# Performance work log

Hardware: AMD Instinct MI355X
Metric: run time of the kernel (lower is better)

The kernel has to match this reference:

```python
import jax, jax.numpy as jnp
import numpy as np

B, N, D, S, H = 64, 4096, 256, 8, 256
ITERS = 3
EPS = 1e-8
SCALE = D ** -0.5


def _ln(x, g, b):
    m = jnp.mean(x, axis=-1, keepdims=True)
    v = jnp.mean((x - m) ** 2, axis=-1, keepdims=True)
    return (x - m) * jax.lax.rsqrt(v + 1e-5) * g + b


def setup_inputs() -> dict:
    key = jax.random.key(0)
    ks = jax.random.split(key, 12)
    s = 0.02
    return {
        'inputs': jax.random.normal(ks[0], (B, N, D), jnp.float32),
        'slot_noise': jax.random.normal(ks[1], (B, S, D), jnp.float32),
        'slots_mean': jax.random.normal(ks[2], (1, 1, D), jnp.float32),
        'slots_logvar': s * jax.random.normal(ks[3], (1, 1, D), jnp.float32),
        'Wq': s * jax.random.normal(ks[4], (D, D), jnp.float32),
        'bq': jnp.zeros((D,), jnp.float32),
        'Wk': s * jax.random.normal(ks[5], (D, D), jnp.float32),
        'bk': jnp.zeros((D,), jnp.float32),
        'Wv': s * jax.random.normal(ks[6], (D, D), jnp.float32),
        'bv': jnp.zeros((D,), jnp.float32),
        'W_ih': s * jax.random.normal(ks[7], (3 * D, D), jnp.float32),
        'b_ih': jnp.zeros((3 * D,), jnp.float32),
        'W_hh': s * jax.random.normal(ks[8], (3 * D, D), jnp.float32),
        'b_hh': jnp.zeros((3 * D,), jnp.float32),
        'W1': s * jax.random.normal(ks[9], (H, D), jnp.float32),
        'b1': jnp.zeros((H,), jnp.float32),
        'W2': s * jax.random.normal(ks[10], (D, H), jnp.float32),
        'b2': jnp.zeros((D,), jnp.float32),
        'g_in': jnp.ones((D,), jnp.float32),
        'bias_in': jnp.zeros((D,), jnp.float32),
        'g_slots': jnp.ones((D,), jnp.float32),
        'bias_slots': jnp.zeros((D,), jnp.float32),
        'g_ff': jnp.ones((D,), jnp.float32),
        'bias_ff': jnp.zeros((D,), jnp.float32),
    }


def reference(inputs, slot_noise, slots_mean, slots_logvar, Wq, bq, Wk, bk, Wv, bv,
              W_ih, b_ih, W_hh, b_hh, W1, b1, W2, b2,
              g_in, bias_in, g_slots, bias_slots, g_ff, bias_ff):
    # slot init: mean + exp(logvar) * noise  (exp(logvar) used as multiplier, as in source)
    slots = slots_mean + jnp.exp(slots_logvar) * slot_noise  # [B,S,D]
    x = _ln(inputs, g_in, bias_in)                            # [B,N,D]
    k = x @ Wk.T + bk
    v = x @ Wv.T + bv
    attn = None
    for _ in range(ITERS):
        slots_prev = slots
        sn = _ln(slots, g_slots, bias_slots)
        q = sn @ Wq.T + bq                                    # [B,S,D]
        dots = jnp.einsum('bid,bjd->bij', q, k) * SCALE       # [B,S,N]
        attn = jax.nn.softmax(dots, axis=1) + EPS             # softmax over slots, no renorm
        updates = jnp.einsum('bjd,bij->bid', v, attn)         # [B,S,D]
        # GRUCell (PyTorch convention)
        gi = updates @ W_ih.T + b_ih                          # [B,S,3D]
        gh = slots_prev @ W_hh.T + b_hh
        i_r, i_z, i_n = jnp.split(gi, 3, axis=-1)
        h_r, h_z, h_n = jnp.split(gh, 3, axis=-1)
        r = jax.nn.sigmoid(i_r + h_r)
        z = jax.nn.sigmoid(i_z + h_z)
        n = jnp.tanh(i_n + r * h_n)
        slots = (1.0 - z) * n + z * slots_prev
        # MLP residual
        sf = _ln(slots, g_ff, bias_ff)
        slots = slots + (jax.nn.relu(sf @ W1.T + b1) @ W2.T + b2)
    return (slots, attn)
```

## Files before the change

kernel.cpp:

```cpp
#include <hip/hip_runtime.h>

typedef unsigned short u16;
typedef __bf16 bf16x8 __attribute__((ext_vector_type(8)));
typedef float f32x4 __attribute__((ext_vector_type(4)));

#define DEV static __device__ __forceinline__

DEV u16 f2bf(float f) {
    unsigned int u = __builtin_bit_cast(unsigned int, f);
    u += 0x7FFFu + ((u >> 16) & 1u);
    return (u16)(u >> 16);
}

DEV bf16x8 frag_ld(const u16* p) {
    return __builtin_bit_cast(bf16x8, *(const uint4*)p);
}

DEV float sigm(float x) { return 1.f / (1.f + __expf(-x)); }

DEV float blo(unsigned u) { return __builtin_bit_cast(float, u << 16); }
DEV float bhi(unsigned u) { return __builtin_bit_cast(float, u & 0xffff0000u); }

__global__ __launch_bounds__(256) void kSetup(
    const float* __restrict__ noise, const float* __restrict__ mean,
    const float* __restrict__ logv, float* __restrict__ slots,
    const float* __restrict__ Wq, const float* __restrict__ Wk,
    const float* __restrict__ bq, const float* __restrict__ bk,
    float* __restrict__ Wqk, float* __restrict__ wbc,
    const float* __restrict__ Wv,  float* __restrict__ WvT,
    const float* __restrict__ Wih, float* __restrict__ WihT,
    const float* __restrict__ Whh, float* __restrict__ WhhT,
    const float* __restrict__ W1,  float* __restrict__ W1T,
    const float* __restrict__ W2,  float* __restrict__ W2T)
{
    __shared__ float tile[32][33];
    const int bid = blockIdx.x, t = threadIdx.x;
    if (bid < 512) {
        const int id = bid * 256 + t;
        const int d = id & 255;
        slots[id] = mean[d] + __expf(logv[d]) * noise[id];
        return;
    }
    if (bid < 770) {
        const int a = bid - 512, e = t;
        if (a < 256) {
            float acc = 0.f;
            for (int d = 0; d < 256; ++d) acc += Wq[(size_t)d * 256 + a] * Wk[(size_t)d * 256 + e];
            Wqk[(size_t)a * 256 + e] = acc;
        } else if (a == 256) {
            float acc = 0.f;
            for (int d = 0; d < 256; ++d) acc += bq[d] * Wk[(size_t)d * 256 + e];
            wbc[e] = acc;
        } else {
            float acc = 0.f;
            for (int d = 0; d < 256; ++d) acc += Wq[(size_t)d * 256 + e] * bk[d];
            wbc[256 + e] = acc;
            if (e == 0) {
                float c0 = 0.f;
                for (int d = 0; d < 256; ++d) c0 += bq[d] * bk[d];
                wbc[512] = c0;
            }
        }
        return;
    }
    const int rb = bid - 770;
    const float* in; float* outp; int R, k;
    if (rb < 64)       { in = Wv;  outp = WvT;  R = 256; k = rb; }
    else if (rb < 256) { in = Wih; outp = WihT; R = 768; k = rb - 64; }
    else if (rb < 448) { in = Whh; outp = WhhT; R = 768; k = rb - 256; }
    else if (rb < 512) { in = W1;  outp = W1T;  R = 256; k = rb - 448; }
    else               { in = W2;  outp = W2T;  R = 256; k = rb - 512; }
    const int bx = k & 7, by = k >> 3;
    const int tx = t & 31, ty = t >> 5;
    const int c0 = bx * 32, r0 = by * 32;
    #pragma unroll
    for (int i = 0; i < 4; ++i)
        tile[ty + i * 8][tx] = in[(size_t)(r0 + ty + i * 8) * 256 + c0 + tx];
    __syncthreads();
    #pragma unroll
    for (int i = 0; i < 4; ++i)
        outp[(size_t)(c0 + ty + i * 8) * R + r0 + tx] = tile[tx][ty + i * 8];
}

__global__ __launch_bounds__(256) void kSn(
    const float* __restrict__ slots, const float* __restrict__ gs, const float* __restrict__ bs,
    const float* __restrict__ Wqk, const float* __restrict__ wbc,
    u16* __restrict__ qo, float* __restrict__ qc)
{
    __shared__ float SN[8][256];
    __shared__ float red2[4][8][64];
    const int t = threadIdx.x;
    const int b = blockIdx.y, seg = blockIdx.x;
    const int w = t >> 6, lane = t & 63;
    #pragma unroll
    for (int rr = 0; rr < 2; ++rr) {
        const int r = w * 2 + rr;
        const int c = lane * 4;
        const float4 x = *(const float4*)(slots + ((size_t)b * 8 + r) * 256 + c);
        float s1 = x.x + x.y + x.z + x.w;
        float s2 = x.x * x.x + x.y * x.y + x.z * x.z + x.w * x.w;
        #pragma unroll
        for (int o = 32; o > 0; o >>= 1) { s1 += __shfl_xor(s1, o); s2 += __shfl_xor(s2, o); }
        const float mu = s1 * (1.f / 256.f);
        const float rs = rsqrtf(s2 * (1.f / 256.f) - mu * mu + 1e-5f);
        const float4 g4 = *(const float4*)(gs + c);
        const float4 b4 = *(const float4*)(bs + c);
        SN[r][c + 0] = (x.x - mu) * rs * g4.x + b4.x;
        SN[r][c + 1] = (x.y - mu) * rs * g4.y + b4.y;
        SN[r][c + 2] = (x.z - mu) * rs * g4.z + b4.z;
        SN[r][c + 3] = (x.w - mu) * rs * g4.w + b4.w;
    }
    __syncthreads();
    const int c = seg * 64 + (t & 63);
    const int p = t >> 6;
    float acc[8] = {};
    #pragma unroll 4
    for (int d = p * 64; d < p * 64 + 64; ++d) {
        const float wq = Wqk[(size_t)d * 256 + c];
        #pragma unroll
        for (int r = 0; r < 8; ++r) acc[r] += wq * SN[r][d];
    }
    #pragma unroll
    for (int r = 0; r < 8; ++r) red2[p][r][t & 63] = acc[r];
    __syncthreads();
    const float bb = wbc[c];
    #pragma unroll
    for (int rr = t >> 6; rr < 8; rr += 4) {
        const float s = red2[0][rr][t & 63] + red2[1][rr][t & 63]
                      + red2[2][rr][t & 63] + red2[3][rr][t & 63];
        qo[((size_t)b * 16 + rr) * 256 + c] = f2bf((s + bb) * 0.0625f);
    }
    if (seg == 0) {
        const int r = t >> 5, l = t & 31;
        float a = 0.f;
        #pragma unroll
        for (int d8 = 0; d8 < 8; ++d8) a += SN[r][l * 8 + d8] * wbc[256 + l * 8 + d8];
        #pragma unroll
        for (int o = 16; o > 0; o >>= 1) a += __shfl_xor(a, o);
        if (l == 0) qc[(size_t)b * 8 + r] = 0.0625f * (a + wbc[512]);
    }
}

template<int FUSE>
__global__ __launch_bounds__(256, 2) void kF(
    const float* __restrict__ X,
    const float* __restrict__ gin, const float* __restrict__ bin,
    const u16* __restrict__ Q,
    const float* __restrict__ qcg,
    u16* __restrict__ XN,
    float* __restrict__ attn_out,
    float* __restrict__ part,
    float* __restrict__ part2,
    int write_attn)
{
    __shared__ __align__(16) float att32[128][8];
    __shared__ float usred[4][8][256];
    __shared__ float sred[4][2][4][16];
    const int tid = threadIdx.x;
    const int w = tid >> 6, lane = tid & 63;
    const int quad = lane >> 4, l16 = lane & 15;
    const int dsg = lane & 31, jg = lane >> 5;
    const int b = blockIdx.y, nt = blockIdx.x;
    const int j0 = nt << 8;
    const size_t rowbase = (size_t)b * 4096 + j0;

    const u16* qb = Q + (size_t)b * 16 * 256;
    bf16x8 qfrag[8];
    #pragma unroll
    for (int k0 = 0; k0 < 8; ++k0)
        qfrag[k0] = frag_ld(qb + l16 * 256 + k0 * 32 + quad * 8);

    float c8[8];
    #pragma unroll
    for (int i = 0; i < 8; ++i) c8[i] = qcg[(size_t)b * 8 + i];

    float4 g4, b4;
    if (FUSE) {
        const int cc = lane << 2;
        g4 = *(const float4*)(gin + cc);
        b4 = *(const float4*)(bin + cc);
    }

    float acc[8][8];
    #pragma unroll
    for (int i = 0; i < 8; ++i)
        #pragma unroll
        for (int e = 0; e < 8; ++e) acc[i][e] = 0.f;
    float sacc[4] = {};

    const u16* xb = XN + rowbase * 256;
    const int qb1 = (quad & 1) << 2;

    for (int st = 0; st < 2; ++st) {
        if (FUSE) {
            const int cc = lane << 2;
            #pragma unroll 4
            for (int i = 0; i < 32; ++i) {
                const size_t gr = rowbase + st * 128 + w * 32 + i;
                const float4 x = *(const float4*)(X + gr * 256 + cc);
                float s1 = x.x + x.y + x.z + x.w;
                float s2 = x.x * x.x + x.y * x.y + x.z * x.z + x.w * x.w;
                #pragma unroll
                for (int o = 32; o > 0; o >>= 1) { s1 += __shfl_xor(s1, o); s2 += __shfl_xor(s2, o); }
                const float mu = s1 * (1.f / 256.f);
                const float rs = rsqrtf(s2 * (1.f / 256.f) - mu * mu + 1e-5f);
                ushort4 pk;
                pk.x = f2bf((x.x - mu) * rs * g4.x + b4.x);
                pk.y = f2bf((x.y - mu) * rs * g4.y + b4.y);
                pk.z = f2bf((x.z - mu) * rs * g4.z + b4.z);
                pk.w = f2bf((x.w - mu) * rs * g4.w + b4.w);
                *(ushort4*)(XN + gr * 256 + cc) = pk;
            }
            asm volatile("s_waitcnt vmcnt(0)" ::: "memory");
        }
        f32x4 dacc[2] = {};
        #pragma unroll
        for (int n2 = 0; n2 < 2; ++n2) {
            const int jsl = w * 32 + n2 * 16 + l16;
            const u16* xrow = xb + ((size_t)(st * 128 + jsl)) * 256;
            #pragma unroll
            for (int k0 = 0; k0 < 8; ++k0) {
                const bf16x8 bfr = frag_ld(xrow + k0 * 32 + quad * 8);
                dacc[n2] = __builtin_amdgcn_mfma_f32_16x16x32_bf16(
                    qfrag[k0], bfr, dacc[n2], 0, 0, 0);
            }
        }
        #pragma unroll
        for (int n2 = 0; n2 < 2; ++n2) {
            const int jsl = w * 32 + n2 * 16 + l16;
            float v[8];
            #pragma unroll
            for (int r = 0; r < 4; ++r) {
                v[qb1 + r]       = dacc[n2][r];
                v[(qb1 ^ 4) + r] = __shfl_xor(dacc[n2][r], 16);
            }
            #pragma unroll
            for (int i = 0; i < 8; ++i) v[i] += c8[i];
            float m = v[0];
            #pragma unroll
            for (int i = 1; i < 8; ++i) m = fmaxf(m, v[i]);
            float s = 0.f;
            #pragma unroll
            for (int i = 0; i < 8; ++i) { v[i] = __expf(v[i] - m); s += v[i]; }
            const float inv = 1.f / s;
            if (quad < 2) {
                float4 av;
                av.x = v[qb1 + 0] * inv + 1e-8f;
                av.y = v[qb1 + 1] * inv + 1e-8f;
                av.z = v[qb1 + 2] * inv + 1e-8f;
                av.w = v[qb1 + 3] * inv + 1e-8f;
                sacc[0] += av.x; sacc[1] += av.y; sacc[2] += av.z; sacc[3] += av.w;
                *(float4*)&att32[jsl][qb1] = av;
                if (write_attn) {
                    attn_out[((size_t)b * 8 + qb1 + 0) * 4096 + j0 + st * 128 + jsl] = av.x;
                    attn_out[((size_t)b * 8 + qb1 + 1) * 4096 + j0 + st * 128 + jsl] = av.y;
                    attn_out[((size_t)b * 8 + qb1 + 2) * 4096 + j0 + st * 128 + jsl] = av.z;
                    attn_out[((size_t)b * 8 + qb1 + 3) * 4096 + j0 + st * 128 + jsl] = av.w;
                }
            }
        }
        #pragma unroll 4
        for (int jj = 0; jj < 16; ++jj) {
            const int jsl = w * 32 + jj * 2 + jg;
            const uint4 raw = *(const uint4*)(xb + ((size_t)(st * 128 + jsl)) * 256 + dsg * 8);
            const float4 a0 = *(const float4*)&att32[jsl][0];
            const float4 a1 = *(const float4*)&att32[jsl][4];
            float xf[8];
            xf[0] = blo(raw.x); xf[1] = bhi(raw.x);
            xf[2] = blo(raw.y); xf[3] = bhi(raw.y);
            xf[4] = blo(raw.z); xf[5] = bhi(raw.z);
            xf[6] = blo(raw.w); xf[7] = bhi(raw.w);
            #pragma unroll
            for (int e = 0; e < 8; ++e) {
                acc[0][e] = fmaf(a0.x, xf[e], acc[0][e]);
                acc[1][e] = fmaf(a0.y, xf[e], acc[1][e]);
                acc[2][e] = fmaf(a0.z, xf[e], acc[2][e]);
                acc[3][e] = fmaf(a0.w, xf[e], acc[3][e]);
                acc[4][e] = fmaf(a1.x, xf[e], acc[4][e]);
                acc[5][e] = fmaf(a1.y, xf[e], acc[5][e]);
                acc[6][e] = fmaf(a1.z, xf[e], acc[6][e]);
                acc[7][e] = fmaf(a1.w, xf[e], acc[7][e]);
            }
        }
    }

    #pragma unroll
    for (int i = 0; i < 8; ++i)
        #pragma unroll
        for (int e = 0; e < 8; ++e) acc[i][e] += __shfl_xor(acc[i][e], 32);
    if (jg == 0) {
        #pragma unroll
        for (int i = 0; i < 8; ++i) {
            float4 lo, hi;
            lo.x = acc[i][0]; lo.y = acc[i][1]; lo.z = acc[i][2]; lo.w = acc[i][3];
            hi.x = acc[i][4]; hi.y = acc[i][5]; hi.z = acc[i][6]; hi.w = acc[i][7];
            *(float4*)&usred[w][i][dsg * 8]     = lo;
            *(float4*)&usred[w][i][dsg * 8 + 4] = hi;
        }
    }
    if (quad < 2) {
        #pragma unroll
        for (int r = 0; r < 4; ++r) sred[w][quad][r][l16] = sacc[r];
    }
    __syncthreads();
    #pragma unroll
    for (int i = 0; i < 8; ++i) {
        const float s = usred[0][i][tid] + usred[1][i][tid]
                      + usred[2][i][tid] + usred[3][i][tid];
        part[(((size_t)nt * 64 + b) * 8 + i) * 256 + tid] = s;
    }
    if (tid < 8) {
        const int q = tid >> 2, r = tid & 3;
        float s = 0.f;
        #pragma unroll
        for (int ww = 0; ww < 4; ++ww)
            #pragma unroll
            for (int l = 0; l < 16; ++l) s += sred[ww][q][r][l];
        part2[((size_t)nt * 64 + b) * 8 + tid] = s;
    }
}

__global__ __launch_bounds__(256) void kB3(
    const float* __restrict__ part, const float* __restrict__ part2,
    const float* __restrict__ WvT, const float* __restrict__ bv,
    const float* __restrict__ sl_in,
    const float* __restrict__ WihT, const float* __restrict__ bih,
    const float* __restrict__ WhhT, const float* __restrict__ bhh,
    const float* __restrict__ W1T, const float* __restrict__ b1,
    const float* __restrict__ W2T, const float* __restrict__ b2,
    const float* __restrict__ gf, const float* __restrict__ bff,
    float* __restrict__ sl_out)
{
    __shared__ float Ul[2][256], Sl[2][256];
    __shared__ float red[2][4][6][256];
    __shared__ float SNl[2][256];
    __shared__ float cw[2][2][4];
    __shared__ float Ssl[2];
    const int t = threadIdx.x;
    const int kp = t >> 6, c = t & 63;
    const int row0 = blockIdx.x * 2;

    #pragma unroll
    for (int r = 0; r < 2; ++r) {
        const int row = row0 + r;
        const int b = row >> 3, s = row & 7;
        float u = 0.f;
        #pragma unroll
        for (int nt = 0; nt < 16; ++nt)
            u += part[(((size_t)nt * 64 + b) * 8 + s) * 256 + t];
        Ul[r][t] = u;
        Sl[r][t] = sl_in[(size_t)row * 256 + t];
    }
    if (t < 2) {
        const int row = row0 + t;
        const int b = row >> 3, s = row & 7;
        float ss = 0.f;
        #pragma unroll
        for (int nt = 0; nt < 16; ++nt) ss += part2[((size_t)nt * 64 + b) * 8 + s];
        Ssl[t] = ss;
    }
    __syncthreads();

    {
        float va[2][4] = {};
        #pragma unroll 4
        for (int dd = 0; dd < 64; ++dd) {
            const int d = kp * 64 + dd;
            const float* wr = WvT + (size_t)d * 256;
            const float u0 = Ul[0][d], u1 = Ul[1][d];
            #pragma unroll
            for (int cg = 0; cg < 4; ++cg) {
                const float wv = wr[cg * 64 + c];
                va[0][cg] += wv * u0;
                va[1][cg] += wv * u1;
            }
        }
        #pragma unroll
        for (int r = 0; r < 2; ++r)
            #pragma unroll
            for (int cg = 0; cg < 4; ++cg)
                red[r][kp][0][cg * 64 + c] = va[r][cg];
    }
    __syncthreads();
    const float bvt = bv[t];
    float upd2[2];
    #pragma unroll
    for (int r = 0; r < 2; ++r)
        upd2[r] = red[r][0][0][t] + red[r][1][0][t] + red[r][2][0][t] + red[r][3][0][t]
                + Ssl[r] * bvt;
    __syncthreads();
    #pragma unroll
    for (int r = 0; r < 2; ++r) Ul[r][t] = upd2[r];
    __syncthreads();

    float ga[2][4][6] = {};
    #pragma unroll 2
    for (int dd = 0; dd < 64; ++dd) {
        const int d = kp * 64 + dd;
        const float* wi = WihT + (size_t)d * 768;
        const float* wh = WhhT + (size_t)d * 768;
        const float u0 = Ul[0][d], u1 = Ul[1][d];
        const float s0 = Sl[0][d], s1 = Sl[1][d];
        #pragma unroll
        for (int cg = 0; cg < 4; ++cg) {
            const int t2 = cg * 64 + c;
            const float wa = wi[t2], wb = wi[256 + t2], wc = wi[512 + t2];
            const float wd = wh[t2], we = wh[256 + t2], wf = wh[512 + t2];
            ga[0][cg][0] += wa * u0; ga[0][cg][1] += wb * u0; ga[0][cg][2] += wc * u0;
            ga[0][cg][3] += wd * s0; ga[0][cg][4] += we * s0; ga[0][cg][5] += wf * s0;
            ga[1][cg][0] += wa * u1; ga[1][cg][1] += wb * u1; ga[1][cg][2] += wc * u1;
            ga[1][cg][3] += wd * s1; ga[1][cg][4] += we * s1; ga[1][cg][5] += wf * s1;
        }
    }
    #pragma unroll
    for (int r = 0; r < 2; ++r)
        #pragma unroll
        for (int cg = 0; cg < 4; ++cg)
            #pragma unroll
            for (int g = 0; g < 6; ++g)
                red[r][kp][g][cg * 64 + c] = ga[r][cg][g];
    __syncthreads();

    const float b_ir = bih[t], b_iz = bih[256 + t], b_in = bih[512 + t];
    const float b_hr = bhh[t], b_hz = bhh[256 + t], b_hn = bhh[512 + t];
    float hnew[2];
    #pragma unroll
    for (int r = 0; r < 2; ++r) {
        float s6[6];
        #pragma unroll
        for (int g = 0; g < 6; ++g)
            s6[g] = red[r][0][g][t] + red[r][1][g][t] + red[r][2][g][t] + red[r][3][g][t];
        const float rg = sigm(s6[0] + b_ir + s6[3] + b_hr);
        const float zg = sigm(s6[1] + b_iz + s6[4] + b_hz);
        const float ng = tanhf(s6[2] + b_in + rg * (s6[5] + b_hn));
        hnew[r] = (1.f - zg) * ng + zg * Sl[r][t];
    }
    #pragma unroll
    for (int r = 0; r < 2; ++r) {
        float s1 = hnew[r], s2 = hnew[r] * hnew[r];
        #pragma unroll
        for (int o = 32; o > 0; o >>= 1) { s1 += __shfl_xor(s1, o); s2 += __shfl_xor(s2, o); }
        if (c == 0) { cw[r][0][kp] = s1; cw[r][1][kp] = s2; }
    }
    __syncthreads();
    const float gft = gf[t], bfft = bff[t];
    #pragma unroll
    for (int r = 0; r < 2; ++r) {
        const float s1 = cw[r][0][0] + cw[r][0][1] + cw[r][0][2] + cw[r][0][3];
        const float s2 = cw[r][1][0] + cw[r][1][1] + cw[r][1][2] + cw[r][1][3];
        const float mu = s1 * (1.f / 256.f);
        const float rs = rsqrtf(s2 * (1.f / 256.f) - mu * mu + 1e-5f);
        SNl[r][t] = (hnew[r] - mu) * rs * gft + bfft;
    }
    __syncthreads();

    {
        float m1[2][4] = {};
        #pragma unroll 4
        for (int dd = 0; dd < 64; ++dd) {
            const int d = kp * 64 + dd;
            const float* wr = W1T + (size_t)d * 256;
            const float n0 = SNl[0][d], n1 = SNl[1][d];
            #pragma unroll
            for (int cg = 0; cg < 4; ++cg) {
                const float wv = wr[cg * 64 + c];
                m1[0][cg] += wv * n0;
                m1[1][cg] += wv * n1;
            }
        }
        #pragma unroll
        for (int r = 0; r < 2; ++r)
            #pragma unroll
            for (int cg = 0; cg < 4; ++cg)
                red[r][kp][0][cg * 64 + c] = m1[r][cg];
    }
    __syncthreads();
    const float b1t = b1[t];
    float h1v[2];
    #pragma unroll
    for (int r = 0; r < 2; ++r)
        h1v[r] = fmaxf(red[r][0][0][t] + red[r][1][0][t] + red[r][2][0][t] + red[r][3][0][t]
                       + b1t, 0.f);
    __syncthreads();
    #pragma unroll
    for (int r = 0; r < 2; ++r) SNl[r][t] = h1v[r];
    __syncthreads();
    {
        float m2[2][4] = {};
        #pragma unroll 4
        for (int dd = 0; dd < 64; ++dd) {
            const int d = kp * 64 + dd;
            const float* wr = W2T + (size_t)d * 256;
            const float x0 = SNl[0][d], x1 = SNl[1][d];
            #pragma unroll
            for (int cg = 0; cg < 4; ++cg) {
                const float wv = wr[cg * 64 + c];
                m2[0][cg] += wv * x0;
                m2[1][cg] += wv * x1;
            }
        }
        #pragma unroll
        for (int r = 0; r < 2; ++r)
            #pragma unroll
            for (int cg = 0; cg < 4; ++cg)
                red[r][kp][1][cg * 64 + c] = m2[r][cg];
    }
    __syncthreads();
    const float b2t = b2[t];
    #pragma unroll
    for (int r = 0; r < 2; ++r) {
        const float o = red[r][0][1][t] + red[r][1][1][t] + red[r][2][1][t] + red[r][3][1][t];
        sl_out[(size_t)(row0 + r) * 256 + t] = hnew[r] + o + b2t;
    }
}

extern "C" void kernel_launch(void* const* d_in, const int* in_sizes, int n_in,
                              void* d_out, int out_size, void* d_ws, size_t ws_size,
                              hipStream_t stream) {
    const float* inputs = (const float*)d_in[0];
    const float* noise  = (const float*)d_in[1];
    const float* smean  = (const float*)d_in[2];
    const float* slogv  = (const float*)d_in[3];
    const float* Wq  = (const float*)d_in[4];
    const float* bq  = (const float*)d_in[5];
    const float* Wk  = (const float*)d_in[6];
    const float* bk  = (const float*)d_in[7];
    const float* Wv  = (const float*)d_in[8];
    const float* bv  = (const float*)d_in[9];
    const float* Wih = (const float*)d_in[10];
    const float* bih = (const float*)d_in[11];
    const float* Whh = (const float*)d_in[12];
    const float* bhh = (const float*)d_in[13];
    const float* W1  = (const float*)d_in[14];
    const float* b1  = (const float*)d_in[15];
    const float* W2  = (const float*)d_in[16];
    const float* b2  = (const float*)d_in[17];
    const float* gin = (const float*)d_in[18];
    const float* bin = (const float*)d_in[19];
    const float* gs  = (const float*)d_in[20];
    const float* bs  = (const float*)d_in[21];
    const float* gf  = (const float*)d_in[22];
    const float* bff = (const float*)d_in[23];

    char* ws = (char*)d_ws;
    u16*  XNw    = (u16*)(ws);
    u16*  qw     = (u16*)(ws + 134217728ull);
    float* slots = (float*)(ws + 134742016ull);
    float* Wqkw  = (float*)(ws + 135266304ull);
    float* wbc   = (float*)(ws + 135528448ull);
    float* qcw   = (float*)(ws + 135532544ull);
    float* WvT   = (float*)(ws + 135536640ull);
    float* WihT  = (float*)(ws + 135798784ull);
    float* WhhT  = (float*)(ws + 136585216ull);
    float* W1T   = (float*)(ws + 137371648ull);
    float* W2T   = (float*)(ws + 137633792ull);
    float* partw = (float*)(ws + 137895936ull);
    float* part2w= (float*)(ws + 146284544ull);

    float* out = (float*)d_out;
    float* attn_out = out + 131072;

    kSetup<<<1346, 256, 0, stream>>>(noise, smean, slogv, slots,
                                     Wq, Wk, bq, bk, Wqkw, wbc,
                                     Wv, WvT, Wih, WihT, Whh, WhhT, W1, W1T, W2, W2T);
    for (int it = 0; it < 3; ++it) {
        kSn<<<dim3(4, 64), 256, 0, stream>>>(slots, gs, bs, Wqkw, wbc, qw, qcw);
        if (it == 0)
            kF<1><<<dim3(16, 64), 256, 0, stream>>>(inputs, gin, bin, qw, qcw, XNw,
                                                    attn_out, partw, part2w, 0);
        else
            kF<0><<<dim3(16, 64), 256, 0, stream>>>(inputs, gin, bin, qw, qcw, XNw,
                                                    attn_out, partw, part2w, it == 2);
        kB3<<<256, 256, 0, stream>>>(partw, part2w, WvT, bv, slots,
                                     WihT, bih, WhhT, bhh, W1T, b1, W2T, b2, gf, bff,
                                     (it == 2) ? out : slots);
    }
}
```

Measured before the change: 715.6 us.

## Fuse per-iteration kernels into one persistent kernel with software grid barriers

```diff
diff --git a/kernel.cpp b/kernel.cpp
--- a/kernel.cpp
+++ b/kernel.cpp
@@ -20,6 +20,26 @@
 
 DEV float blo(unsigned u) { return __builtin_bit_cast(float, u << 16); }
 DEV float bhi(unsigned u) { return __builtin_bit_cast(float, u & 0xffff0000u); }
+
+#define NBLK 512
+
+DEV void gridSync(unsigned* bar) {
+    __threadfence();
+    __syncthreads();
+    if (threadIdx.x == 0) {
+        const unsigned g = __hip_atomic_load(bar + 1, __ATOMIC_RELAXED, __HIP_MEMORY_SCOPE_AGENT);
+        const unsigned a = __hip_atomic_fetch_add(bar, 1u, __ATOMIC_ACQ_REL, __HIP_MEMORY_SCOPE_AGENT);
+        if (a == NBLK - 1u) {
+            __hip_atomic_store(bar, 0u, __ATOMIC_RELAXED, __HIP_MEMORY_SCOPE_AGENT);
+            __hip_atomic_fetch_add(bar + 1, 1u, __ATOMIC_RELEASE, __HIP_MEMORY_SCOPE_AGENT);
+        } else {
+            while (__hip_atomic_load(bar + 1, __ATOMIC_ACQUIRE, __HIP_MEMORY_SCOPE_AGENT) == g)
+                __builtin_amdgcn_s_sleep(1);
+        }
+    }
+    __syncthreads();
+    __threadfence();
+}
 
 __global__ __launch_bounds__(256) void kSetup(
     const float* __restrict__ noise, const float* __restrict__ mean,
@@ -31,11 +51,13 @@
     const float* __restrict__ Wih, float* __restrict__ WihT,
     const float* __restrict__ Whh, float* __restrict__ WhhT,
     const float* __restrict__ W1,  float* __restrict__ W1T,
-    const float* __restrict__ W2,  float* __restrict__ W2T)
+    const float* __restrict__ W2,  float* __restrict__ W2T,
+    unsigned* __restrict__ bar)
 {
     __shared__ float tile[32][33];
     const int bid = blockIdx.x, t = threadIdx.x;
     if (bid < 512) {
+        if (bid == 0 && t < 2) bar[t] = 0u;
         const int id = bid * 256 + t;
         const int d = id & 255;
         slots[id] = mean[d] + __expf(logv[d]) * noise[id];
@@ -82,435 +104,381 @@
         outp[(size_t)(c0 + ty + i * 8) * R + r0 + tx] = tile[tx][ty + i * 8];
 }
 
-__global__ __launch_bounds__(256) void kSn(
-    const float* __restrict__ slots, const float* __restrict__ gs, const float* __restrict__ bs,
+struct SnS { float SN[8][256]; float red2[4][8][64]; };
+struct FS  { float att32[128][8]; float usred[4][8][256]; float sred[4][2][4][16]; };
+struct B3S { float Ul[256], Sl[256], SNl[256]; float red[4][6][256];
+             float cw[2][4]; float Ssl; };
+
+__global__ __launch_bounds__(256, 2) void kLoop(
+    float* __restrict__ slots, const float* __restrict__ gs, const float* __restrict__ bs,
     const float* __restrict__ Wqk, const float* __restrict__ wbc,
-    u16* __restrict__ qo, float* __restrict__ qc)
-{
-    __shared__ float SN[8][256];
-    __shared__ float red2[4][8][64];
-    const int t = threadIdx.x;
-    const int b = blockIdx.y, seg = blockIdx.x;
-    const int w = t >> 6, lane = t & 63;
-    #pragma unroll
-    for (int rr = 0; rr < 2; ++rr) {
-        const int r = w * 2 + rr;
-        const int c = lane * 4;
-        const float4 x = *(const float4*)(slots + ((size_t)b * 8 + r) * 256 + c);
-        float s1 = x.x + x.y + x.z + x.w;
-        float s2 = x.x * x.x + x.y * x.y + x.z * x.z + x.w * x.w;
-        #pragma unroll
-        for (int o = 32; o > 0; o >>= 1) { s1 += __shfl_xor(s1, o); s2 += __shfl_xor(s2, o); }
-        const float mu = s1 * (1.f / 256.f);
-        const float rs = rsqrtf(s2 * (1.f / 256.f) - mu * mu + 1e-5f);
-        const float4 g4 = *(const float4*)(gs + c);
-        const float4 b4 = *(const float4*)(bs + c);
-        SN[r][c + 0] = (x.x - mu) * rs * g4.x + b4.x;
-        SN[r][c + 1] = (x.y - mu) * rs * g4.y + b4.y;
-        SN[r][c + 2] = (x.z - mu) * rs * g4.z + b4.z;
-        SN[r][c + 3] = (x.w - mu) * rs * g4.w + b4.w;
-    }
-    __syncthreads();
-    const int c = seg * 64 + (t & 63);
-    const int p = t >> 6;
-    float acc[8] = {};
-    #pragma unroll 4
-    for (int d = p * 64; d < p * 64 + 64; ++d) {
-        const float wq = Wqk[(size_t)d * 256 + c];
-        #pragma unroll
-        for (int r = 0; r < 8; ++r) acc[r] += wq * SN[r][d];
-    }
-    #pragma unroll
-    for (int r = 0; r < 8; ++r) red2[p][r][t & 63] = acc[r];
-    __syncthreads();
-    const float bb = wbc[c];
-    #pragma unroll
-    for (int rr = t >> 6; rr < 8; rr += 4) {
-        const float s = red2[0][rr][t & 63] + red2[1][rr][t & 63]
-                      + red2[2][rr][t & 63] + red2[3][rr][t & 63];
-        qo[((size_t)b * 16 + rr) * 256 + c] = f2bf((s + bb) * 0.0625f);
-    }
-    if (seg == 0) {
-        const int r = t >> 5, l = t & 31;
-        float a = 0.f;
-        #pragma unroll
-        for (int d8 = 0; d8 < 8; ++d8) a += SN[r][l * 8 + d8] * wbc[256 + l * 8 + d8];
-        #pragma unroll
-        for (int o = 16; o > 0; o >>= 1) a += __shfl_xor(a, o);
-        if (l == 0) qc[(size_t)b * 8 + r] = 0.0625f * (a + wbc[512]);
-    }
-}
-
-template<int FUSE>
-__global__ __launch_bounds__(256, 2) void kF(
-    const float* __restrict__ X,
-    const float* __restrict__ gin, const float* __restrict__ bin,
-    const u16* __restrict__ Q,
-    const float* __restrict__ qcg,
-    u16* __restrict__ XN,
-    float* __restrict__ attn_out,
-    float* __restrict__ part,
-    float* __restrict__ part2,
-    int write_attn)
-{
-    __shared__ __align__(16) float att32[128][8];
-    __shared__ float usred[4][8][256];
-    __shared__ float sred[4][2][4][16];
-    const int tid = threadIdx.x;
-    const int w = tid >> 6, lane = tid & 63;
-    const int quad = lane >> 4, l16 = lane & 15;
-    const int dsg = lane & 31, jg = lane >> 5;
-    const int b = blockIdx.y, nt = blockIdx.x;
-    const int j0 = nt << 8;
-    const size_t rowbase = (size_t)b * 4096 + j0;
-
-    const u16* qb = Q + (size_t)b * 16 * 256;
-    bf16x8 qfrag[8];
-    #pragma unroll
-    for (int k0 = 0; k0 < 8; ++k0)
-        qfrag[k0] = frag_ld(qb + l16 * 256 + k0 * 32 + quad * 8);
-
-    float c8[8];
-    #pragma unroll
-    for (int i = 0; i < 8; ++i) c8[i] = qcg[(size_t)b * 8 + i];
-
-    float4 g4, b4;
-    if (FUSE) {
-        const int cc = lane << 2;
-        g4 = *(const float4*)(gin + cc);
-        b4 = *(const float4*)(bin + cc);
-    }
-
-    float acc[8][8];
-    #pragma unroll
-    for (int i = 0; i < 8; ++i)
-        #pragma unroll
-        for (int e = 0; e < 8; ++e) acc[i][e] = 0.f;
-    float sacc[4] = {};
-
-    const u16* xb = XN + rowbase * 256;
-    const int qb1 = (quad & 1) << 2;
-
-    for (int st = 0; st < 2; ++st) {
-        if (FUSE) {
-            const int cc = lane << 2;
-            #pragma unroll 4
-            for (int i = 0; i < 32; ++i) {
-                const size_t gr = rowbase + st * 128 + w * 32 + i;
-                const float4 x = *(const float4*)(X + gr * 256 + cc);
-                float s1 = x.x + x.y + x.z + x.w;
-                float s2 = x.x * x.x + x.y * x.y + x.z * x.z + x.w * x.w;
-                #pragma unroll
-                for (int o = 32; o > 0; o >>= 1) { s1 += __shfl_xor(s1, o); s2 += __shfl_xor(s2, o); }
-                const float mu = s1 * (1.f / 256.f);
-                const float rs = rsqrtf(s2 * (1.f / 256.f) - mu * mu + 1e-5f);
-                ushort4 pk;
-                pk.x = f2bf((x.x - mu) * rs * g4.x + b4.x);
-                pk.y = f2bf((x.y - mu) * rs * g4.y + b4.y);
-                pk.z = f2bf((x.z - mu) * rs * g4.z + b4.z);
-                pk.w = f2bf((x.w - mu) * rs * g4.w + b4.w);
-                *(ushort4*)(XN + gr * 256 + cc) = pk;
-            }
-            asm volatile("s_waitcnt vmcnt(0)" ::: "memory");
-        }
-        f32x4 dacc[2] = {};
-        #pragma unroll
-        for (int n2 = 0; n2 < 2; ++n2) {
-            const int jsl = w * 32 + n2 * 16 + l16;
-            const u16* xrow = xb + ((size_t)(st * 128 + jsl)) * 256;
-            #pragma unroll
-            for (int k0 = 0; k0 < 8; ++k0) {
-                const bf16x8 bfr = frag_ld(xrow + k0 * 32 + quad * 8);
-                dacc[n2] = __builtin_amdgcn_mfma_f32_16x16x32_bf16(
-                    qfrag[k0], bfr, dacc[n2], 0, 0, 0);
-            }
-        }
-        #pragma unroll
-        for (int n2 = 0; n2 < 2; ++n2) {
-            const int jsl = w * 32 + n2 * 16 + l16;
-            float v[8];
-            #pragma unroll
-            for (int r = 0; r < 4; ++r) {
-                v[qb1 + r]       = dacc[n2][r];
-                v[(qb1 ^ 4) + r] = __shfl_xor(dacc[n2][r], 16);
-            }
-            #pragma unroll
-            for (int i = 0; i < 8; ++i) v[i] += c8[i];
-            float m = v[0];
-            #pragma unroll
-            for (int i = 1; i < 8; ++i) m = fmaxf(m, v[i]);
-            float s = 0.f;
-            #pragma unroll
-            for (int i = 0; i < 8; ++i) { v[i] = __expf(v[i] - m); s += v[i]; }
-            const float inv = 1.f / s;
-            if (quad < 2) {
-                float4 av;
-                av.x = v[qb1 + 0] * inv + 1e-8f;
-                av.y = v[qb1 + 1] * inv + 1e-8f;
-                av.z = v[qb1 + 2] * inv + 1e-8f;
-                av.w = v[qb1 + 3] * inv + 1e-8f;
-                sacc[0] += av.x; sacc[1] += av.y; sacc[2] += av.z; sacc[3] += av.w;
-                *(float4*)&att32[jsl][qb1] = av;
-                if (write_attn) {
-                    attn_out[((size_t)b * 8 + qb1 + 0) * 4096 + j0 + st * 128 + jsl] = av.x;
-                    attn_out[((size_t)b * 8 + qb1 + 1) * 4096 + j0 + st * 128 + jsl] = av.y;
-                    attn_out[((size_t)b * 8 + qb1 + 2) * 4096 + j0 + st * 128 + jsl] = av.z;
-                    attn_out[((size_t)b * 8 + qb1 + 3) * 4096 + j0 + st * 128 + jsl] = av.w;
-                }
-            }
-        }
-        #pragma unroll 4
-        for (int jj = 0; jj < 16; ++jj) {
-            const int jsl = w * 32 + jj * 2 + jg;
-            const uint4 raw = *(const uint4*)(xb + ((size_t)(st * 128 + jsl)) * 256 + dsg * 8);
-            const float4 a0 = *(const float4*)&att32[jsl][0];
-            const float4 a1 = *(const float4*)&att32[jsl][4];
-            float xf[8];
-            xf[0] = blo(raw.x); xf[1] = bhi(raw.x);
-            xf[2] = blo(raw.y); xf[3] = bhi(raw.y);
-            xf[4] = blo(raw.z); xf[5] = bhi(raw.z);
-            xf[6] = blo(raw.w); xf[7] = bhi(raw.w);
-            #pragma unroll
-            for (int e = 0; e < 8; ++e) {
-                acc[0][e] = fmaf(a0.x, xf[e], acc[0][e]);
-                acc[1][e] = fmaf(a0.y, xf[e], acc[1][e]);
-                acc[2][e] = fmaf(a0.z, xf[e], acc[2][e]);
-                acc[3][e] = fmaf(a0.w, xf[e], acc[3][e]);
-                acc[4][e] = fmaf(a1.x, xf[e], acc[4][e]);
-                acc[5][e] = fmaf(a1.y, xf[e], acc[5][e]);
-                acc[6][e] = fmaf(a1.z, xf[e], acc[6][e]);
-                acc[7][e] = fmaf(a1.w, xf[e], acc[7][e]);
-            }
-        }
-    }
-
-    #pragma unroll
-    for (int i = 0; i < 8; ++i)
-        #pragma unroll
-        for (int e = 0; e < 8; ++e) acc[i][e] += __shfl_xor(acc[i][e], 32);
-    if (jg == 0) {
-        #pragma unroll
-        for (int i = 0; i < 8; ++i) {
-            float4 lo, hi;
-            lo.x = acc[i][0]; lo.y = acc[i][1]; lo.z = acc[i][2]; lo.w = acc[i][3];
-            hi.x = acc[i][4]; hi.y = acc[i][5]; hi.z = acc[i][6]; hi.w = acc[i][7];
-            *(float4*)&usred[w][i][dsg * 8]     = lo;
-            *(float4*)&usred[w][i][dsg * 8 + 4] = hi;
-        }
-    }
-    if (quad < 2) {
-        #pragma unroll
-        for (int r = 0; r < 4; ++r) sred[w][quad][r][l16] = sacc[r];
-    }
-    __syncthreads();
-    #pragma unroll
-    for (int i = 0; i < 8; ++i) {
-        const float s = usred[0][i][tid] + usred[1][i][tid]
-                      + usred[2][i][tid] + usred[3][i][tid];
-        part[(((size_t)nt * 64 + b) * 8 + i) * 256 + tid] = s;
-    }
-    if (tid < 8) {
-        const int q = tid >> 2, r = tid & 3;
-        float s = 0.f;
-        #pragma unroll
-        for (int ww = 0; ww < 4; ++ww)
-            #pragma unroll
-            for (int l = 0; l < 16; ++l) s += sred[ww][q][r][l];
-        part2[((size_t)nt * 64 + b) * 8 + tid] = s;
-    }
-}
-
-__global__ __launch_bounds__(256) void kB3(
-    const float* __restrict__ part, const float* __restrict__ part2,
+    u16* __restrict__ qw, float* __restrict__ qc,
+    const float* __restrict__ X, const float* __restrict__ gin, const float* __restrict__ bin,
+    u16* __restrict__ XN, float* __restrict__ attn_out,
+    float* __restrict__ part, float* __restrict__ part2,
     const float* __restrict__ WvT, const float* __restrict__ bv,
-    const float* __restrict__ sl_in,
     const float* __restrict__ WihT, const float* __restrict__ bih,
     const float* __restrict__ WhhT, const float* __restrict__ bhh,
     const float* __restrict__ W1T, const float* __restrict__ b1,
     const float* __restrict__ W2T, const float* __restrict__ b2,
     const float* __restrict__ gf, const float* __restrict__ bff,
-    float* __restrict__ sl_out)
+    float* __restrict__ out, unsigned* bar)
 {
-    __shared__ float Ul[2][256], Sl[2][256];
-    __shared__ float red[2][4][6][256];
-    __shared__ float SNl[2][256];
-    __shared__ float cw[2][2][4];
-    __shared__ float Ssl[2];
-    const int t = threadIdx.x;
-    const int kp = t >> 6, c = t & 63;
-    const int row0 = blockIdx.x * 2;
-
-    #pragma unroll
-    for (int r = 0; r < 2; ++r) {
-        const int row = row0 + r;
-        const int b = row >> 3, s = row & 7;
-        float u = 0.f;
-        #pragma unroll
-        for (int nt = 0; nt < 16; ++nt)
-            u += part[(((size_t)nt * 64 + b) * 8 + s) * 256 + t];
-        Ul[r][t] = u;
-        Sl[r][t] = sl_in[(size_t)row * 256 + t];
-    }
-    if (t < 2) {
-        const int row = row0 + t;
-        const int b = row >> 3, s = row & 7;
-        float ss = 0.f;
-        #pragma unroll
-        for (int nt = 0; nt < 16; ++nt) ss += part2[((size_t)nt * 64 + b) * 8 + s];
-        Ssl[t] = ss;
-    }
-    __syncthreads();
-
-    {
-        float va[2][4] = {};
-        #pragma unroll 4
-        for (int dd = 0; dd < 64; ++dd) {
-            const int d = kp * 64 + dd;
-            const float* wr = WvT + (size_t)d * 256;
-            const float u0 = Ul[0][d], u1 = Ul[1][d];
+    __shared__ __align__(16) char smem_[38912];
+    const int blk = blockIdx.x;
+    const int tid = threadIdx.x;
+
+    for (int it = 0; it < 3; ++it) {
+        if (blk < 256) {
+            SnS& sm = *reinterpret_cast<SnS*>(smem_);
+            const int b = blk >> 2, seg = blk & 3;
+            const int t = tid;
+            const int w = t >> 6, lane = t & 63;
             #pragma unroll
-            for (int cg = 0; cg < 4; ++cg) {
-                const float wv = wr[cg * 64 + c];
-                va[0][cg] += wv * u0;
-                va[1][cg] += wv * u1;
+            for (int rr = 0; rr < 2; ++rr) {
+                const int r = w * 2 + rr;
+                const int c = lane * 4;
+                const float4 x = *(const float4*)(slots + ((size_t)b * 8 + r) * 256 + c);
+                float s1 = x.x + x.y + x.z + x.w;
+                float s2 = x.x * x.x + x.y * x.y + x.z * x.z + x.w * x.w;
+                #pragma unroll
+                for (int o = 32; o > 0; o >>= 1) { s1 += __shfl_xor(s1, o); s2 += __shfl_xor(s2, o); }
+                const float mu = s1 * (1.f / 256.f);
+                const float rs = rsqrtf(s2 * (1.f / 256.f) - mu * mu + 1e-5f);
+                const float4 g4 = *(const float4*)(gs + c);
+                const float4 b4 = *(const float4*)(bs + c);
+                sm.SN[r][c + 0] = (x.x - mu) * rs * g4.x + b4.x;
+                sm.SN[r][c + 1] = (x.y - mu) * rs * g4.y + b4.y;
+                sm.SN[r][c + 2] = (x.z - mu) * rs * g4.z + b4.z;
+                sm.SN[r][c + 3] = (x.w - mu) * rs * g4.w + b4.w;
+            }
+            __syncthreads();
+            const int c = seg * 64 + (t & 63);
+            const int p = t >> 6;
+            float acc[8] = {};
+            #pragma unroll 4
+            for (int d = p * 64; d < p * 64 + 64; ++d) {
+                const float wq = Wqk[(size_t)d * 256 + c];
+                #pragma unroll
+                for (int r = 0; r < 8; ++r) acc[r] += wq * sm.SN[r][d];
+            }
+            #pragma unroll
+            for (int r = 0; r < 8; ++r) sm.red2[p][r][t & 63] = acc[r];
+            __syncthreads();
+            const float bb = wbc[c];
+            #pragma unroll
+            for (int rr = t >> 6; rr < 8; rr += 4) {
+                const float s = sm.red2[0][rr][t & 63] + sm.red2[1][rr][t & 63]
+                              + sm.red2[2][rr][t & 63] + sm.red2[3][rr][t & 63];
+                qw[((size_t)b * 16 + rr) * 256 + c] = f2bf((s + bb) * 0.0625f);
+            }
+            if (seg == 0) {
+                const int r = t >> 5, l = t & 31;
+                float a = 0.f;
+                #pragma unroll
+                for (int d8 = 0; d8 < 8; ++d8) a += sm.SN[r][l * 8 + d8] * wbc[256 + l * 8 + d8];
+                #pragma unroll
+                for (int o = 16; o > 0; o >>= 1) a += __shfl_xor(a, o);
+                if (l == 0) qc[(size_t)b * 8 + r] = 0.0625f * (a + wbc[512]);
             }
         }
-        #pragma unroll
-        for (int r = 0; r < 2; ++r)
-            #pragma unroll
-            for (int cg = 0; cg < 4; ++cg)
-                red[r][kp][0][cg * 64 + c] = va[r][cg];
-    }
-    __syncthreads();
-    const float bvt = bv[t];
-    float upd2[2];
-    #pragma unroll
-    for (int r = 0; r < 2; ++r)
-        upd2[r] = red[r][0][0][t] + red[r][1][0][t] + red[r][2][0][t] + red[r][3][0][t]
-                + Ssl[r] * bvt;
-    __syncthreads();
-    #pragma unroll
-    for (int r = 0; r < 2; ++r) Ul[r][t] = upd2[r];
-    __syncthreads();
-
-    float ga[2][4][6] = {};
-    #pragma unroll 2
-    for (int dd = 0; dd < 64; ++dd) {
-        const int d = kp * 64 + dd;
-        const float* wi = WihT + (size_t)d * 768;
-        const float* wh = WhhT + (size_t)d * 768;
-        const float u0 = Ul[0][d], u1 = Ul[1][d];
-        const float s0 = Sl[0][d], s1 = Sl[1][d];
-        #pragma unroll
-        for (int cg = 0; cg < 4; ++cg) {
-            const int t2 = cg * 64 + c;
-            const float wa = wi[t2], wb = wi[256 + t2], wc = wi[512 + t2];
-            const float wd = wh[t2], we = wh[256 + t2], wf = wh[512 + t2];
-            ga[0][cg][0] += wa * u0; ga[0][cg][1] += wb * u0; ga[0][cg][2] += wc * u0;
-            ga[0][cg][3] += wd * s0; ga[0][cg][4] += we * s0; ga[0][cg][5] += wf * s0;
-            ga[1][cg][0] += wa * u1; ga[1][cg][1] += wb * u1; ga[1][cg][2] += wc * u1;
-            ga[1][cg][3] += wd * s1; ga[1][cg][4] += we * s1; ga[1][cg][5] += wf * s1;
+        gridSync(bar);
+
+        {
+            FS& sm = *reinterpret_cast<FS*>(smem_);
+            const int w = tid >> 6, lane = tid & 63;
+            const int quad = lane >> 4, l16 = lane & 15;
+            const int dsg = lane & 31, jg = lane >> 5;
+            const int qb1 = (quad & 1) << 2;
+            const int write_attn = (it == 2);
+            float4 g4, b4;
+            if (it == 0) {
+                const int cc = lane << 2;
+                g4 = *(const float4*)(gin + cc);
+                b4 = *(const float4*)(bin + cc);
+            }
+            #pragma unroll 1
+            for (int u = 0; u < 2; ++u) {
+                const int unit = (u << 9) + blk;
+                const int nt = unit >> 6, b = unit & 63;
+                const int j0 = nt << 8;
+                const size_t rowbase = (size_t)b * 4096 + j0;
+                const u16* qptr = qw + (size_t)b * 16 * 256;
+                bf16x8 qfrag[8];
+                #pragma unroll
+                for (int k0 = 0; k0 < 8; ++k0)
+                    qfrag[k0] = frag_ld(qptr + l16 * 256 + k0 * 32 + quad * 8);
+                float c8[8];
+                #pragma unroll
+                for (int i = 0; i < 8; ++i) c8[i] = qc[(size_t)b * 8 + i];
+
+                float acc[8][8];
+                #pragma unroll
+                for (int i = 0; i < 8; ++i)
+                    #pragma unroll
+                    for (int e = 0; e < 8; ++e) acc[i][e] = 0.f;
+                float sacc[4] = {};
+                const u16* xb = XN + rowbase * 256;
+
+                for (int st = 0; st < 2; ++st) {
+                    if (it == 0) {
+                        const int cc = lane << 2;
+                        #pragma unroll 4
+                        for (int i = 0; i < 32; ++i) {
+                            const size_t gr = rowbase + st * 128 + w * 32 + i;
+                            const float4 x = *(const float4*)(X + gr * 256 + cc);
+                            float s1 = x.x + x.y + x.z + x.w;
+                            float s2 = x.x * x.x + x.y * x.y + x.z * x.z + x.w * x.w;
+                            #pragma unroll
+                            for (int o = 32; o > 0; o >>= 1) { s1 += __shfl_xor(s1, o); s2 += __shfl_xor(s2, o); }
+                            const float mu = s1 * (1.f / 256.f);
+                            const float rs = rsqrtf(s2 * (1.f / 256.f) - mu * mu + 1e-5f);
+                            ushort4 pk;
+                            pk.x = f2bf((x.x - mu) * rs * g4.x + b4.x);
+                            pk.y = f2bf((x.y - mu) * rs * g4.y + b4.y);
+                            pk.z = f2bf((x.z - mu) * rs * g4.z + b4.z);
+                            pk.w = f2bf((x.w - mu) * rs * g4.w + b4.w);
+                            *(ushort4*)(XN + gr * 256 + cc) = pk;
+                        }
+                        asm volatile("s_waitcnt vmcnt(0)" ::: "memory");
+                    }
+                    f32x4 dacc[2] = {};
+                    #pragma unroll
+                    for (int n2 = 0; n2 < 2; ++n2) {
+                        const int jsl = w * 32 + n2 * 16 + l16;
+                        const u16* xrow = xb + ((size_t)(st * 128 + jsl)) * 256;
+                        #pragma unroll
+                        for (int k0 = 0; k0 < 8; ++k0) {
+                            const bf16x8 bfr = frag_ld(xrow + k0 * 32 + quad * 8);
+                            dacc[n2] = __builtin_amdgcn_mfma_f32_16x16x32_bf16(
+                                qfrag[k0], bfr, dacc[n2], 0, 0, 0);
+                        }
+                    }
+                    #pragma unroll
+                    for (int n2 = 0; n2 < 2; ++n2) {
+                        const int jsl = w * 32 + n2 * 16 + l16;
+                        float v[8];
+                        #pragma unroll
+                        for (int r = 0; r < 4; ++r) {
+                            v[qb1 + r]       = dacc[n2][r];
+                            v[(qb1 ^ 4) + r] = __shfl_xor(dacc[n2][r], 16);
+                        }
+                        #pragma unroll
+                        for (int i = 0; i < 8; ++i) v[i] += c8[i];
+                        float m = v[0];
+                        #pragma unroll
+                        for (int i = 1; i < 8; ++i) m = fmaxf(m, v[i]);
+                        float s = 0.f;
+                        #pragma unroll
+                        for (int i = 0; i < 8; ++i) { v[i] = __expf(v[i] - m); s += v[i]; }
+                        const float inv = 1.f / s;
+                        if (quad < 2) {
+                            float4 av;
+                            av.x = v[qb1 + 0] * inv + 1e-8f;
+                            av.y = v[qb1 + 1] * inv + 1e-8f;
+                            av.z = v[qb1 + 2] * inv + 1e-8f;
+                            av.w = v[qb1 + 3] * inv + 1e-8f;
+                            sacc[0] += av.x; sacc[1] += av.y; sacc[2] += av.z; sacc[3] += av.w;
+                            *(float4*)&sm.att32[jsl][qb1] = av;
+                            if (write_attn) {
+                                attn_out[((size_t)b * 8 + qb1 + 0) * 4096 + j0 + st * 128 + jsl] = av.x;
+                                attn_out[((size_t)b * 8 + qb1 + 1) * 4096 + j0 + st * 128 + jsl] = av.y;
+                                attn_out[((size_t)b * 8 + qb1 + 2) * 4096 + j0 + st * 128 + jsl] = av.z;
+                                attn_out[((size_t)b * 8 + qb1 + 3) * 4096 + j0 + st * 128 + jsl] = av.w;
+                            }
+                        }
+                    }
+                    #pragma unroll 4
+                    for (int jj = 0; jj < 16; ++jj) {
+                        const int jsl = w * 32 + jj * 2 + jg;
+                        const uint4 raw = *(const uint4*)(xb + ((size_t)(st * 128 + jsl)) * 256 + dsg * 8);
+                        const float4 a0 = *(const float4*)&sm.att32[jsl][0];
+                        const float4 a1 = *(const float4*)&sm.att32[jsl][4];
+                        float xf[8];
+                        xf[0] = blo(raw.x); xf[1] = bhi(raw.x);
+                        xf[2] = blo(raw.y); xf[3] = bhi(raw.y);
+                        xf[4] = blo(raw.z); xf[5] = bhi(raw.z);
+                        xf[6] = blo(raw.w); xf[7] = bhi(raw.w);
+                        #pragma unroll
+                        for (int e = 0; e < 8; ++e) {
+                            acc[0][e] = fmaf(a0.x, xf[e], acc[0][e]);
+                            acc[1][e] = fmaf(a0.y, xf[e], acc[1][e]);
+                            acc[2][e] = fmaf(a0.z, xf[e], acc[2][e]);
+                            acc[3][e] = fmaf(a0.w, xf[e], acc[3][e]);
+                            acc[4][e] = fmaf(a1.x, xf[e], acc[4][e]);
+                            acc[5][e] = fmaf(a1.y, xf[e], acc[5][e]);
+                            acc[6][e] = fmaf(a1.z, xf[e], acc[6][e]);
+                            acc[7][e] = fmaf(a1.w, xf[e], acc[7][e]);
+                        }
+                    }
+                }
+                #pragma unroll
+                for (int i = 0; i < 8; ++i)
+                    #pragma unroll
+                    for (int e = 0; e < 8; ++e) acc[i][e] += __shfl_xor(acc[i][e], 32);
+                __syncthreads();
+                if (jg == 0) {
+                    #pragma unroll
+                    for (int i = 0; i < 8; ++i) {
+                        float4 lo, hi;
+                        lo.x = acc[i][0]; lo.y = acc[i][1]; lo.z = acc[i][2]; lo.w = acc[i][3];
+                        hi.x = acc[i][4]; hi.y = acc[i][5]; hi.z = acc[i][6]; hi.w = acc[i][7];
+                        *(float4*)&sm.usred[w][i][dsg * 8]     = lo;
+                        *(float4*)&sm.usred[w][i][dsg * 8 + 4] = hi;
+                    }
+                }
+                if (quad < 2) {
+                    #pragma unroll
+                    for (int r = 0; r < 4; ++r) sm.sred[w][quad][r][l16] = sacc[r];
+                }
+                __syncthreads();
+                #pragma unroll
+                for (int i = 0; i < 8; ++i) {
+                    const float s = sm.usred[0][i][tid] + sm.usred[1][i][tid]
+                                  + sm.usred[2][i][tid] + sm.usred[3][i][tid];
+                    part[(((size_t)nt * 64 + b) * 8 + i) * 256 + tid] = s;
+                }
+                if (tid < 8) {
+                    const int q = tid >> 2, r = tid & 3;
+                    float s = 0.f;
+                    #pragma unroll
+                    for (int ww = 0; ww < 4; ++ww)
+                        #pragma unroll
+                        for (int l = 0; l < 16; ++l) s += sm.sred[ww][q][r][l];
+                    part2[((size_t)nt * 64 + b) * 8 + tid] = s;
+                }
+            }
         }
-    }
-    #pragma unroll
-    for (int r = 0; r < 2; ++r)
-        #pragma unroll
-        for (int cg = 0; cg < 4; ++cg)
+        gridSync(bar);
+
+        {
+            B3S& sm = *reinterpret_cast<B3S*>(smem_);
+            const int t = tid;
+            const int kp = t >> 6, c = t & 63;
+            const int row = blk;
+            const int b = row >> 3, s = row & 7;
+            float* sl_out = (it == 2) ? out : slots;
+            {
+                float uacc = 0.f;
+                #pragma unroll
+                for (int nt = 0; nt < 16; ++nt)
+                    uacc += part[(((size_t)nt * 64 + b) * 8 + s) * 256 + t];
+                sm.Ul[t] = uacc;
+                sm.Sl[t] = slots[(size_t)row * 256 + t];
+                if (t == 0) {
+                    float ss = 0.f;
+                    #pragma unroll
+                    for (int nt = 0; nt < 16; ++nt) ss += part2[((size_t)nt * 64 + b) * 8 + s];
+                    sm.Ssl = ss;
+                }
+            }
+            __syncthreads();
+            {
+                float va[4] = {};
+                #pragma unroll 4
+                for (int dd = 0; dd < 64; ++dd) {
+                    const int d = kp * 64 + dd;
+                    const float* wr = WvT + (size_t)d * 256;
+                    const float u0 = sm.Ul[d];
+                    #pragma unroll
+                    for (int cg = 0; cg < 4; ++cg) va[cg] += wr[cg * 64 + c] * u0;
+                }
+                #pragma unroll
+                for (int cg = 0; cg < 4; ++cg) sm.red[kp][0][cg * 64 + c] = va[cg];
+            }
+            __syncthreads();
+            const float updv = sm.red[0][0][t] + sm.red[1][0][t] + sm.red[2][0][t] + sm.red[3][0][t]
+                             + sm.Ssl * bv[t];
+            __syncthreads();
+            sm.Ul[t] = updv;
+            __syncthreads();
+            {
+                float ga[4][6] = {};
+                #pragma unroll 2
+                for (int dd = 0; dd < 64; ++dd) {
+                    const int d = kp * 64 + dd;
+                    const float* wi = WihT + (size_t)d * 768;
+                    const float* wh = WhhT + (size_t)d * 768;
+                    const float u0 = sm.Ul[d], s0 = sm.Sl[d];
+                    #pragma unroll
+                    for (int cg = 0; cg < 4; ++cg) {
+                        const int t2 = cg * 64 + c;
+                        ga[cg][0] += wi[t2] * u0;
+                        ga[cg][1] += wi[256 + t2] * u0;
+                        ga[cg][2] += wi[512 + t2] * u0;
+                        ga[cg][3] += wh[t2] * s0;
+                        ga[cg][4] += wh[256 + t2] * s0;
+                        ga[cg][5] += wh[512 + t2] * s0;
+                    }
+                }
+                #pragma unroll
+                for (int cg = 0; cg < 4; ++cg)
+                    #pragma unroll
+                    for (int g = 0; g < 6; ++g)
+                        sm.red[kp][g][cg * 64 + c] = ga[cg][g];
+            }
+            __syncthreads();
+            float s6[6];
             #pragma unroll
             for (int g = 0; g < 6; ++g)
-                red[r][kp][g][cg * 64 + c] = ga[r][cg][g];
-    __syncthreads();
-
-    const float b_ir = bih[t], b_iz = bih[256 + t], b_in = bih[512 + t];
-    const float b_hr = bhh[t], b_hz = bhh[256 + t], b_hn = bhh[512 + t];
-    float hnew[2];
-    #pragma unroll
-    for (int r = 0; r < 2; ++r) {
-        float s6[6];
-        #pragma unroll
-        for (int g = 0; g < 6; ++g)
-            s6[g] = red[r][0][g][t] + red[r][1][g][t] + red[r][2][g][t] + red[r][3][g][t];
-        const float rg = sigm(s6[0] + b_ir + s6[3] + b_hr);
-        const float zg = sigm(s6[1] + b_iz + s6[4] + b_hz);
-        const float ng = tanhf(s6[2] + b_in + rg * (s6[5] + b_hn));
-        hnew[r] = (1.f - zg) * ng + zg * Sl[r][t];
-    }
-    #pragma unroll
-    for (int r = 0; r < 2; ++r) {
-        float s1 = hnew[r], s2 = hnew[r] * hnew[r];
-        #pragma unroll
-        for (int o = 32; o > 0; o >>= 1) { s1 += __shfl_xor(s1, o); s2 += __shfl_xor(s2, o); }
-        if (c == 0) { cw[r][0][kp] = s1; cw[r][1][kp] = s2; }
-    }
-    __syncthreads();
-    const float gft = gf[t], bfft = bff[t];
-    #pragma unroll
-    for (int r = 0; r < 2; ++r) {
-        const float s1 = cw[r][0][0] + cw[r][0][1] + cw[r][0][2] + cw[r][0][3];
-        const float s2 = cw[r][1][0] + cw[r][1][1] + cw[r][1][2] + cw[r][1][3];
-        const float mu = s1 * (1.f / 256.f);
-        const float rs = rsqrtf(s2 * (1.f / 256.f) - mu * mu + 1e-5f);
-        SNl[r][t] = (hnew[r] - mu) * rs * gft + bfft;
-    }
-    __syncthreads();
-
-    {
-        float m1[2][4] = {};
-        #pragma unroll 4
-        for (int dd = 0; dd < 64; ++dd) {
-            const int d = kp * 64 + dd;
-            const float* wr = W1T + (size_t)d * 256;
-            const float n0 = SNl[0][d], n1 = SNl[1][d];
-            #pragma unroll
-            for (int cg = 0; cg < 4; ++cg) {
-                const float wv = wr[cg * 64 + c];
-                m1[0][cg] += wv * n0;
-                m1[1][cg] += wv * n1;
-            }
+                s6[g] = sm.red[0][g][t] + sm.red[1][g][t] + sm.red[2][g][t] + sm.red[3][g][t];
+            const float rg = sigm(s6[0] + bih[t] + s6[3] + bhh[t]);
+            const float zg = sigm(s6[1] + bih[256 + t] + s6[4] + bhh[256 + t]);
+            const float ng = tanhf(s6[2] + bih[512 + t] + rg * (s6[5] + bhh[512 + t]));
+            const float hnew = (1.f - zg) * ng + zg * sm.Sl[t];
+            {
+                float s1 = hnew, s2 = hnew * hnew;
+                #pragma unroll
+                for (int o = 32; o > 0; o >>= 1) { s1 += __shfl_xor(s1, o); s2 += __shfl_xor(s2, o); }
+                if ((t & 63) == 0) { sm.cw[0][kp] = s1; sm.cw[1][kp] = s2; }
+            }
+            __syncthreads();
+            {
+                const float sum1 = sm.cw[0][0] + sm.cw[0][1] + sm.cw[0][2] + sm.cw[0][3];
+                const float sum2 = sm.cw[1][0] + sm.cw[1][1] + sm.cw[1][2] + sm.cw[1][3];
+                const float mu = sum1 * (1.f / 256.f);
+                const float rs = rsqrtf(sum2 * (1.f / 256.f) - mu * mu + 1e-5f);
+                sm.SNl[t] = (hnew - mu) * rs * gf[t] + bff[t];
+            }
+            __syncthreads();
+            {
+                float m1[4] = {};
+                #pragma unroll 4
+                for (int dd = 0; dd < 64; ++dd) {
+                    const int d = kp * 64 + dd;
+                    const float* wr = W1T + (size_t)d * 256;
+                    const float n0 = sm.SNl[d];
+                    #pragma unroll
+                    for (int cg = 0; cg < 4; ++cg) m1[cg] += wr[cg * 64 + c] * n0;
+                }
+                #pragma unroll
+                for (int cg = 0; cg < 4; ++cg) sm.red[kp][0][cg * 64 + c] = m1[cg];
+            }
+            __syncthreads();
+            const float h1 = fmaxf(sm.red[0][0][t] + sm.red[1][0][t] + sm.red[2][0][t]
+                                   + sm.red[3][0][t] + b1[t], 0.f);
+            __syncthreads();
+            sm.SNl[t] = h1;
+            __syncthreads();
+            {
+                float m2[4] = {};
+                #pragma unroll 4
+                for (int dd = 0; dd < 64; ++dd) {
+                    const int d = kp * 64 + dd;
+                    const float* wr = W2T + (size_t)d * 256;
+                    const float x0 = sm.SNl[d];
+                    #pragma unroll
+                    for (int cg = 0; cg < 4; ++cg) m2[cg] += wr[cg * 64 + c] * x0;
+                }
+                #pragma unroll
+                for (int cg = 0; cg < 4; ++cg) sm.red[kp][0][cg * 64 + c] = m2[cg];
+            }
+            __syncthreads();
+            const float o = sm.red[0][0][t] + sm.red[1][0][t] + sm.red[2][0][t] + sm.red[3][0][t]
+                          + b2[t];
+            sl_out[(size_t)row * 256 + t] = hnew + o;
         }
-        #pragma unroll
-        for (int r = 0; r < 2; ++r)
-            #pragma unroll
-            for (int cg = 0; cg < 4; ++cg)
-                red[r][kp][0][cg * 64 + c] = m1[r][cg];
-    }
-    __syncthreads();
-    const float b1t = b1[t];
-    float h1v[2];
-    #pragma unroll
-    for (int r = 0; r < 2; ++r)
-        h1v[r] = fmaxf(red[r][0][0][t] + red[r][1][0][t] + red[r][2][0][t] + red[r][3][0][t]
-                       + b1t, 0.f);
-    __syncthreads();
-    #pragma unroll
-    for (int r = 0; r < 2; ++r) SNl[r][t] = h1v[r];
-    __syncthreads();
-    {
-        float m2[2][4] = {};
-        #pragma unroll 4
-        for (int dd = 0; dd < 64; ++dd) {
-            const int d = kp * 64 + dd;
-            const float* wr = W2T + (size_t)d * 256;
-            const float x0 = SNl[0][d], x1 = SNl[1][d];
-            #pragma unroll
-            for (int cg = 0; cg < 4; ++cg) {
-                const float wv = wr[cg * 64 + c];
-                m2[0][cg] += wv * x0;
-                m2[1][cg] += wv * x1;
-            }
-        }
-        #pragma unroll
-        for (int r = 0; r < 2; ++r)
-            #pragma unroll
-            for (int cg = 0; cg < 4; ++cg)
-                red[r][kp][1][cg * 64 + c] = m2[r][cg];
-    }
-    __syncthreads();
-    const float b2t = b2[t];
-    #pragma unroll
-    for (int r = 0; r < 2; ++r) {
-        const float o = red[r][0][1][t] + red[r][1][1][t] + red[r][2][1][t] + red[r][3][1][t];
-        sl_out[(size_t)(row0 + r) * 256 + t] = hnew[r] + o + b2t;
+        if (it < 2) gridSync(bar);
     }
 }
 
@@ -556,23 +524,17 @@
     float* W2T   = (float*)(ws + 137633792ull);
     float* partw = (float*)(ws + 137895936ull);
     float* part2w= (float*)(ws + 146284544ull);
+    unsigned* barw = (unsigned*)(ws + 146317312ull);
 
     float* out = (float*)d_out;
     float* attn_out = out + 131072;
 
     kSetup<<<1346, 256, 0, stream>>>(noise, smean, slogv, slots,
                                      Wq, Wk, bq, bk, Wqkw, wbc,
-                                     Wv, WvT, Wih, WihT, Whh, WhhT, W1, W1T, W2, W2T);
-    for (int it = 0; it < 3; ++it) {
-        kSn<<<dim3(4, 64), 256, 0, stream>>>(slots, gs, bs, Wqkw, wbc, qw, qcw);
-        if (it == 0)
-            kF<1><<<dim3(16, 64), 256, 0, stream>>>(inputs, gin, bin, qw, qcw, XNw,
-                                                    attn_out, partw, part2w, 0);
-        else
-            kF<0><<<dim3(16, 64), 256, 0, stream>>>(inputs, gin, bin, qw, qcw, XNw,
-                                                    attn_out, partw, part2w, it == 2);
-        kB3<<<256, 256, 0, stream>>>(partw, part2w, WvT, bv, slots,
-                                     WihT, bih, WhhT, bhh, W1T, b1, W2T, b2, gf, bff,
-                                     (it == 2) ? out : slots);
-    }
+                                     Wv, WvT, Wih, WihT, Whh, WhhT, W1, W1T, W2, W2T,
+                                     barw);
+    kLoop<<<NBLK, 256, 0, stream>>>(slots, gs, bs, Wqkw, wbc, qw, qcw,
+                                    inputs, gin, bin, XNw, attn_out, partw, part2w,
+                                    WvT, bv, WihT, bih, WhhT, bhh, W1T, b1, W2T, b2,
+                                    gf, bff, out, barw);
 }
```

New measurement: 2.181 ms. 3.05x slower.
